# Optimization experiments

Hardware: AMD Instinct MI355X
Metric: run time of the kernel (lower is better)

The kernel has to match this reference:

```python
import jax, jax.numpy as jnp
import numpy as np
from jax import lax

HEADS = 8
DIM_HEAD = 64
INNER = HEADS * DIM_HEAD  # 512
LOG_SCALE_MAX = float(np.log(100.0))  # clamp for clamp_exp (SwinV2-style max temperature 1/0.01)
EPS_NORM = 1e-12  # F.normalize eps
EPS_LN = 1e-5


def setup_inputs() -> dict:
    key = jax.random.key(0)
    ks = jax.random.split(key, 6)
    b, c, h, w = 2, 256, 48, 48
    x = jax.random.normal(ks[0], (b, c, h, w), jnp.float32)
    w_in = jax.random.normal(ks[1], (3 * INNER, c), jnp.float32) * (c ** -0.5)
    b_in = jnp.zeros((3 * INNER,), jnp.float32)
    # learnable log-scale, init log(d_head ** -0.5), per head
    softmax_scale = jnp.full((HEADS, 1, 1), float(np.log(DIM_HEAD ** -0.5)), jnp.float32)
    w_dw = jax.random.normal(ks[2], (INNER, 1, 3, 3), jnp.float32) * (1.0 / 3.0)
    w_pw = jax.random.normal(ks[3], (2 * c, INNER), jnp.float32) * (INNER ** -0.5)
    gamma = jnp.full((2 * c,), 1e-3, jnp.float32)  # norm init_weight=0.001
    beta = jnp.zeros((2 * c,), jnp.float32)
    return {"x": x, "w_in": w_in, "b_in": b_in, "softmax_scale": softmax_scale,
            "w_dw": w_dw, "w_pw": w_pw, "gamma": gamma, "beta": beta}


def _l2norm(t):
    n = jnp.sqrt(jnp.sum(t * t, axis=-1, keepdims=True))
    return t / jnp.maximum(n, EPS_NORM)


def reference(x, w_in, b_in, softmax_scale, w_dw, w_pw, gamma, beta):
    b, c, h, w = x.shape
    s = h * w
    # proj_in: 1x1 conv then 'b (h c) x y -> b h x y c'
    y = jnp.einsum('bchw,oc->bohw', x, w_in) + b_in[None, :, None, None]
    y = y.reshape(b, HEADS, 3 * DIM_HEAD, h, w).transpose(0, 1, 3, 4, 2)  # b H x y (3*dh)
    y = y.reshape(b, HEADS, s, 3 * DIM_HEAD)
    q, k, v = jnp.split(y, 3, axis=-1)  # each [b, H, s, dh]
    # scaled cosine attention
    qn, kn = _l2norm(q), _l2norm(k)
    scale = jnp.exp(jnp.minimum(softmax_scale, LOG_SCALE_MAX))  # clamp_exp, [H,1,1]
    sim = jnp.einsum('bhid,bhjd->bhij', qn, kn) * scale[None]
    attn = jax.nn.softmax(sim, axis=-1)
    out = jnp.einsum('bhij,bhjd->bhid', attn, v)  # [b,H,s,dh]
    # unsplit heads -> 'b (h w) c' -> 'b c h w'
    update = out.transpose(0, 2, 1, 3).reshape(b, s, INNER)
    update = update.transpose(0, 2, 1).reshape(b, INNER, h, w)
    # proj_out: depthwise 3x3 (no bias) + pointwise 1x1 (no bias)
    dw = lax.conv_general_dilated(update, w_dw, (1, 1), 'SAME',
                                  feature_group_count=INNER,
                                  dimension_numbers=('NCHW', 'OIHW', 'NCHW'))
    pw = jnp.einsum('bchw,oc->bohw', dw, w_pw)  # [b, 2c, h, w]
    # channelwise layernorm with small init weight (norm_scales_and_shifts)
    mu = jnp.mean(pw, axis=1, keepdims=True)
    var = jnp.var(pw, axis=1, keepdims=True)
    normed = (pw - mu) * lax.rsqrt(var + EPS_LN)
    normed = normed * gamma[None, :, None, None] + beta[None, :, None, None]
    scales, shifts = jnp.split(normed, 2, axis=1)  # each [b, c, h, w]
    return shifts + x * scales
```

## Files before the change

kernel.cpp:

```cpp
#include <hip/hip_runtime.h>

#define B_ 2
#define C_ 256
#define S_ 2304
#define DH_ 64
#define O3_ 1536
#define INNER_ 512
#define LOGSMAX 4.605170185988092f
#define LOG2E 1.4426950408889634f

typedef __attribute__((ext_vector_type(8))) short short8;
typedef __attribute__((ext_vector_type(4))) float f32x4;
typedef __attribute__((ext_vector_type(16))) float f32x16;
typedef __attribute__((ext_vector_type(4))) unsigned short us4;
typedef __attribute__((ext_vector_type(2))) unsigned u32x2;
typedef __attribute__((ext_vector_type(4))) unsigned u32x4;
typedef __bf16 bf16x8 __attribute__((ext_vector_type(8)));

__device__ __forceinline__ unsigned short f2bf(float f) {
  unsigned u = __builtin_bit_cast(unsigned, f);
  u += 0x7FFFu + ((u >> 16) & 1u);
  return (unsigned short)(u >> 16);
}
__device__ __forceinline__ float bf2f(unsigned short h) {
  return __builtin_bit_cast(float, (unsigned)h << 16);
}
__device__ __forceinline__ bf16x8 as_bf(short8 v) {
  return __builtin_bit_cast(bf16x8, v);
}
__device__ __forceinline__ float fexp2(float x) {
#if __has_builtin(__builtin_amdgcn_exp2f)
  return __builtin_amdgcn_exp2f(x);
#else
  return __expf(x * 0.6931471805599453f);
#endif
}
__device__ __forceinline__ float frcp(float x) {
#if __has_builtin(__builtin_amdgcn_rcpf)
  return __builtin_amdgcn_rcpf(x);
#else
  return 1.f / x;
#endif
}
__device__ __forceinline__ unsigned pack_hi16(unsigned b, unsigned a) {
  return __builtin_amdgcn_perm(b, a, 0x07060302u);
}
__device__ __forceinline__ unsigned pack_lo16(unsigned b, unsigned a) {
  return __builtin_amdgcn_perm(b, a, 0x05040100u);
}

__global__ __launch_bounds__(256) void k_prep(const float* __restrict__ x,
                                              const float* __restrict__ w_in,
                                              const float* __restrict__ w_pw,
                                              unsigned short* __restrict__ xT,
                                              unsigned short* __restrict__ w_inb,
                                              unsigned short* __restrict__ w_pwb) {
  __shared__ float tile[64][65];
  int blk = blockIdx.x;
  int t = threadIdx.x;
  if (blk < 288) {
    int p0 = (blk % 36) * 64, c0 = ((blk / 36) % 4) * 64, b = blk / 144;
    const float* xb = x + (size_t)b * C_ * S_;
#pragma unroll
    for (int i = 0; i < 16; i++) {
      int c = i * 4 + (t >> 6);
      int p = t & 63;
      tile[c][p] = xb[(size_t)(c0 + c) * S_ + p0 + p];
    }
    __syncthreads();
    unsigned short* xTb = xT + (size_t)b * S_ * C_;
#pragma unroll
    for (int i = 0; i < 16; i++) {
      int p = i * 4 + (t >> 6);
      int c = t & 63;
      xTb[(size_t)(p0 + p) * C_ + c0 + c] = f2bf(tile[c][p]);
    }
  } else if (blk < 288 + 1536) {
    int i = (blk - 288) * 256 + t;
    w_inb[i] = f2bf(w_in[i]);
  } else {
    int i = (blk - 1824) * 256 + t;
    w_pwb[i] = f2bf(w_pw[i]);
  }
}

__global__ __launch_bounds__(256) void k_gemm_qkv(const unsigned short* __restrict__ A,
                                                  const unsigned short* __restrict__ BT,
                                                  const float* __restrict__ b_in,
                                                  const float* __restrict__ ss,
                                                  unsigned short* __restrict__ qn,
                                                  unsigned short* __restrict__ kn,
                                                  unsigned short* __restrict__ vv) {
  __shared__ __align__(16) unsigned short As[64][72];
  __shared__ __align__(16) unsigned short Bs[128][72];
  int t = threadIdx.x;
  int lane = t & 63, wv = t >> 6;
  int quad = lane >> 4, r15 = lane & 15;
  int by = blockIdx.y;
  int m0 = by * 64, n0 = blockIdx.x * 128;
  int b = blockIdx.z;
  const unsigned short* BTb = BT + (size_t)b * S_ * C_;

  f32x4 acc[4][2] = {};

  int srA = t >> 2, scA = (t & 3) * 16;
  int srB = t >> 1, scB = (t & 1) * 32;
  const unsigned short* ag = A + (size_t)(m0 + srA) * C_ + scA;
  const unsigned short* bg = BTb + (size_t)(n0 + srB) * C_ + scB;

  for (int k0 = 0; k0 < C_; k0 += 64) {
    short8 a0 = *(const short8*)(ag + k0);
    short8 a1 = *(const short8*)(ag + k0 + 8);
    short8 b0 = *(const short8*)(bg + k0);
    short8 b1 = *(const short8*)(bg + k0 + 8);
    short8 b2 = *(const short8*)(bg + k0 + 16);
    short8 b3 = *(const short8*)(bg + k0 + 24);
    __syncthreads();
    *(short8*)&As[srA][scA] = a0;
    *(short8*)&As[srA][scA + 8] = a1;
    *(short8*)&Bs[srB][scB] = b0;
    *(short8*)&Bs[srB][scB + 8] = b1;
    *(short8*)&Bs[srB][scB + 16] = b2;
    *(short8*)&Bs[srB][scB + 24] = b3;
    __syncthreads();
#pragma unroll
    for (int ks = 0; ks < 2; ks++) {
      short8 af[4], bfr[2];
#pragma unroll
      for (int i = 0; i < 4; i++) af[i] = *(const short8*)&As[i * 16 + r15][ks * 32 + quad * 8];
#pragma unroll
      for (int j = 0; j < 2; j++) bfr[j] = *(const short8*)&Bs[wv * 32 + j * 16 + r15][ks * 32 + quad * 8];
#pragma unroll
      for (int i = 0; i < 4; i++)
#pragma unroll
        for (int j = 0; j < 2; j++)
          acc[i][j] = __builtin_amdgcn_mfma_f32_16x16x32_bf16(as_bf(af[i]), as_bf(bfr[j]), acc[i][j], 0, 0, 0);
    }
  }

  int h = by / 3, seg = by - h * 3;
  int bh = b * 8 + h;
  f32x4 bi[4];
#pragma unroll
  for (int i = 0; i < 4; i++) bi[i] = *(const f32x4*)&b_in[m0 + i * 16 + quad * 4];
  float bv[4][2][4];
  float ssq0 = 0.f, ssq1 = 0.f;
#pragma unroll
  for (int i = 0; i < 4; i++)
#pragma unroll
    for (int rr = 0; rr < 4; rr++) {
      float v0 = acc[i][0][rr] + bi[i][rr];
      float v1 = acc[i][1][rr] + bi[i][rr];
      bv[i][0][rr] = v0;
      bv[i][1][rr] = v1;
      ssq0 += v0 * v0;
      ssq1 += v1 * v1;
    }
  float inv0 = 1.f, inv1 = 1.f;
  if (seg < 2) {
    float sc = (seg == 0) ? __expf(fminf(ss[h], LOGSMAX)) * LOG2E : 1.f;
    ssq0 += __shfl_xor(ssq0, 16);
    ssq0 += __shfl_xor(ssq0, 32);
    ssq1 += __shfl_xor(ssq1, 16);
    ssq1 += __shfl_xor(ssq1, 32);
    inv0 = sc / fmaxf(sqrtf(ssq0), 1e-12f);
    inv1 = sc / fmaxf(sqrtf(ssq1), 1e-12f);
  }
  unsigned short* dst = (seg == 0 ? qn : (seg == 1 ? kn : vv)) + (size_t)bh * S_ * DH_;
#pragma unroll
  for (int i = 0; i < 4; i++)
#pragma unroll
    for (int j = 0; j < 2; j++) {
      float iv = j ? inv1 : inv0;
      us4 o = {f2bf(bv[i][j][0] * iv), f2bf(bv[i][j][1] * iv),
               f2bf(bv[i][j][2] * iv), f2bf(bv[i][j][3] * iv)};
      int p = n0 + wv * 32 + j * 16 + r15;
      *(us4*)&dst[(size_t)p * DH_ + i * 16 + quad * 4] = o;
    }
}

__global__ __launch_bounds__(256) void k_gemm(const unsigned short* __restrict__ A,
                                              const unsigned short* __restrict__ BT,
                                              float* __restrict__ outp,
                                              int M, int N, int K) {
  __shared__ __align__(16) unsigned short As[64][72];
  __shared__ __align__(16) unsigned short Bs[128][72];
  int t = threadIdx.x;
  int lane = t & 63, wv = t >> 6;
  int quad = lane >> 4, r15 = lane & 15;
  int m0 = blockIdx.y * 64, n0 = blockIdx.x * 128;
  int b = blockIdx.z;
  const unsigned short* BTb = BT + (size_t)b * N * K;

  f32x4 acc[4][2] = {};

  int srA = t >> 2, scA = (t & 3) * 16;
  int srB = t >> 1, scB = (t & 1) * 32;
  const unsigned short* ag = A + (size_t)(m0 + srA) * K + scA;
  const unsigned short* bg = BTb + (size_t)(n0 + srB) * K + scB;

  for (int k0 = 0; k0 < K; k0 += 64) {
    short8 a0 = *(const short8*)(ag + k0);
    short8 a1 = *(const short8*)(ag + k0 + 8);
    short8 b0 = *(const short8*)(bg + k0);
    short8 b1 = *(const short8*)(bg + k0 + 8);
    short8 b2 = *(const short8*)(bg + k0 + 16);
    short8 b3 = *(const short8*)(bg + k0 + 24);
    __syncthreads();
    *(short8*)&As[srA][scA] = a0;
    *(short8*)&As[srA][scA + 8] = a1;
    *(short8*)&Bs[srB][scB] = b0;
    *(short8*)&Bs[srB][scB + 8] = b1;
    *(short8*)&Bs[srB][scB + 16] = b2;
    *(short8*)&Bs[srB][scB + 24] = b3;
    __syncthreads();
#pragma unroll
    for (int ks = 0; ks < 2; ks++) {
      short8 af[4], bfr[2];
#pragma unroll
      for (int i = 0; i < 4; i++) af[i] = *(const short8*)&As[i * 16 + r15][ks * 32 + quad * 8];
#pragma unroll
      for (int j = 0; j < 2; j++) bfr[j] = *(const short8*)&Bs[wv * 32 + j * 16 + r15][ks * 32 + quad * 8];
#pragma unroll
      for (int i = 0; i < 4; i++)
#pragma unroll
        for (int j = 0; j < 2; j++)
          acc[i][j] = __builtin_amdgcn_mfma_f32_16x16x32_bf16(as_bf(af[i]), as_bf(bfr[j]), acc[i][j], 0, 0, 0);
    }
  }
  float* Cb = outp + (size_t)b * M * N;
#pragma unroll
  for (int i = 0; i < 4; i++)
#pragma unroll
    for (int j = 0; j < 2; j++)
#pragma unroll
      for (int rr = 0; rr < 4; rr++) {
        int row = m0 + i * 16 + quad * 4 + rr;
        int col = n0 + wv * 32 + j * 16 + r15;
        Cb[(size_t)row * N + col] = acc[i][j][rr];
      }
}

__global__ __launch_bounds__(256) void k_attn(const unsigned short* __restrict__ qn,
                                              const unsigned short* __restrict__ kn,
                                              const unsigned short* __restrict__ vv,
                                              const float* __restrict__ ss,
                                              unsigned short* __restrict__ attnp,
                                              float* __restrict__ lp) {
  __shared__ __align__(16) unsigned short Ks[64][72];
  __shared__ __align__(16) unsigned short Vs[64][72];
  __shared__ __align__(16) unsigned short Ps[4][32][76];
  int t = threadIdx.x;
  int w = t >> 6;
  int lane = t & 63;
  int l31 = lane & 31, hi = lane >> 5;
  int bh = blockIdx.z;
  int q0 = blockIdx.x * 128 + w * 32;
  int split = blockIdx.y;
  int ktbase = split * 12;
  const unsigned short* qb = qn + (size_t)bh * S_ * DH_;
  const unsigned short* kb = kn + (size_t)bh * S_ * DH_;
  const unsigned short* vb = vv + (size_t)bh * S_ * DH_;
  float shift2 = __expf(fminf(ss[bh & 7], LOGSMAX)) * LOG2E;

  const unsigned short* qrow = qb + (size_t)(q0 + l31) * DH_ + hi * 8;
  short8 qf[4];
#pragma unroll
  for (int ks = 0; ks < 4; ks++) qf[ks] = *(const short8*)(qrow + ks * 16);

  const f32x16 z16 = {};
  f32x16 O0 = z16, O1 = z16;
  float l_part = 0.f;

  int srow = t >> 2;
  int scol = (t & 3) * 16;
  const unsigned short* kg = kb + ((size_t)(ktbase * 64) + srow) * DH_ + scol;

  int dp = w * 8 + ((t & 63) >> 3);
  int koct = t & 7;
  const unsigned* vg32 = (const unsigned*)vb + ((size_t)(ktbase * 64 + koct * 8)) * 32 + dp;

  short8 kr0 = *(const short8*)(kg);
  short8 kr1 = *(const short8*)(kg + 8);
  unsigned lv[8];
#pragma unroll
  for (int kk = 0; kk < 8; kk++) lv[kk] = vg32[(size_t)kk * 32];

  for (int i = 0; i < 12; i++) {
    __syncthreads();
    *(short8*)&Ks[srow][scol] = kr0;
    *(short8*)&Ks[srow][scol + 8] = kr1;
    {
      u32x4 ev = {pack_lo16(lv[1], lv[0]), pack_lo16(lv[3], lv[2]),
                  pack_lo16(lv[5], lv[4]), pack_lo16(lv[7], lv[6])};
      u32x4 od = {pack_hi16(lv[1], lv[0]), pack_hi16(lv[3], lv[2]),
                  pack_hi16(lv[5], lv[4]), pack_hi16(lv[7], lv[6])};
      *(u32x4*)&Vs[2 * dp][koct * 8] = ev;
      *(u32x4*)&Vs[2 * dp + 1][koct * 8] = od;
    }
    __syncthreads();
    if (i < 11) {
      size_t koff = (size_t)(i + 1) * 64 * DH_;
      kr0 = *(const short8*)(kg + koff);
      kr1 = *(const short8*)(kg + koff + 8);
      const unsigned* vg = vg32 + (size_t)(i + 1) * 64 * 32;
#pragma unroll
      for (int kk = 0; kk < 8; kk++) lv[kk] = vg[(size_t)kk * 32];
    }
    f32x16 sc0, sc1;
    {
      short8 a0 = *(const short8*)&Ks[l31][hi * 8];
      short8 a1 = *(const short8*)&Ks[32 + l31][hi * 8];
      sc0 = __builtin_amdgcn_mfma_f32_32x32x16_bf16(as_bf(a0), as_bf(qf[0]), z16, 0, 0, 0);
      sc1 = __builtin_amdgcn_mfma_f32_32x32x16_bf16(as_bf(a1), as_bf(qf[0]), z16, 0, 0, 0);
    }
#pragma unroll
    for (int ks = 1; ks < 4; ks++) {
      short8 a0 = *(const short8*)&Ks[l31][ks * 16 + hi * 8];
      short8 a1 = *(const short8*)&Ks[32 + l31][ks * 16 + hi * 8];
      sc0 = __builtin_amdgcn_mfma_f32_32x32x16_bf16(as_bf(a0), as_bf(qf[ks]), sc0, 0, 0, 0);
      sc1 = __builtin_amdgcn_mfma_f32_32x32x16_bf16(as_bf(a1), as_bf(qf[ks]), sc1, 0, 0, 0);
    }
    float lsum = 0.f;
#pragma unroll
    for (int mt = 0; mt < 2; mt++) {
      const f32x16& s = mt ? sc1 : sc0;
#pragma unroll
      for (int g = 0; g < 4; g++) {
        float e0 = fexp2(s[g * 4 + 0] - shift2);
        float e1 = fexp2(s[g * 4 + 1] - shift2);
        float e2 = fexp2(s[g * 4 + 2] - shift2);
        float e3 = fexp2(s[g * 4 + 3] - shift2);
        lsum += (e0 + e1) + (e2 + e3);
        unsigned u0 = __builtin_bit_cast(unsigned, e0) + 0x8000u;
        unsigned u1 = __builtin_bit_cast(unsigned, e1) + 0x8000u;
        unsigned u2 = __builtin_bit_cast(unsigned, e2) + 0x8000u;
        unsigned u3 = __builtin_bit_cast(unsigned, e3) + 0x8000u;
        u32x2 pk = {pack_hi16(u1, u0), pack_hi16(u3, u2)};
        *(u32x2*)&Ps[w][l31][mt * 32 + g * 8 + hi * 4] = pk;
      }
    }
    l_part += lsum;
#pragma unroll
    for (int ks = 0; ks < 4; ks++) {
      short8 pb = *(const short8*)&Ps[w][l31][ks * 16 + hi * 8];
      short8 va0 = *(const short8*)&Vs[l31][ks * 16 + hi * 8];
      short8 va1 = *(const short8*)&Vs[32 + l31][ks * 16 + hi * 8];
      O0 = __builtin_amdgcn_mfma_f32_32x32x16_bf16(as_bf(va0), as_bf(pb), O0, 0, 0, 0);
      O1 = __builtin_amdgcn_mfma_f32_32x32x16_bf16(as_bf(va1), as_bf(pb), O1, 0, 0, 0);
    }
  }
  float l = l_part + __shfl_xor(l_part, 32);
  if (hi == 0) lp[((size_t)(split * 16 + bh)) * S_ + q0 + l31] = l;
  unsigned short* orow = attnp + (((size_t)(split * 16 + bh)) * S_ + q0 + l31) * DH_;
#pragma unroll
  for (int mt = 0; mt < 2; mt++) {
    const f32x16& O = mt ? O1 : O0;
#pragma unroll
    for (int g = 0; g < 4; g++) {
      us4 o4 = {f2bf(O[g * 4 + 0]), f2bf(O[g * 4 + 1]), f2bf(O[g * 4 + 2]), f2bf(O[g * 4 + 3])};
      *(us4*)&orow[mt * 32 + g * 8 + hi * 4] = o4;
    }
  }
}

__global__ __launch_bounds__(256) void k_dwconv(const unsigned short* __restrict__ attnp,
                                                const float* __restrict__ lp,
                                                const float* __restrict__ w_dw,
                                                unsigned short* __restrict__ dwb) {
  int t = threadIdx.x;
  int d = t & 63;
  int pj = t >> 6;
  int p = blockIdx.x * 4 + pj;
  int bh = blockIdx.y;
  int b = bh >> 3, h = bh & 7;
  int yy = p / 48, xx = p % 48;
  const unsigned short* a0 = attnp + (size_t)bh * S_ * DH_ + d;
  const unsigned short* a1 = attnp + ((size_t)(16 + bh)) * S_ * DH_ + d;
  const unsigned short* a2 = attnp + ((size_t)(32 + bh)) * S_ * DH_ + d;
  const float* l0 = lp + (size_t)bh * S_;
  const float* l1 = lp + (size_t)(16 + bh) * S_;
  const float* l2 = lp + (size_t)(32 + bh) * S_;
  int ch = h * 64 + d;
  float w[9];
#pragma unroll
  for (int i = 0; i < 9; i++) w[i] = w_dw[ch * 9 + i];
  float acc = 0.f;
#pragma unroll
  for (int dy = -1; dy <= 1; dy++) {
    int y2 = yy + dy;
    if (y2 < 0 || y2 >= 48) continue;
#pragma unroll
    for (int dx = -1; dx <= 1; dx++) {
      int x2 = xx + dx;
      if (x2 < 0 || x2 >= 48) continue;
      int p2 = y2 * 48 + x2;
      float rl = frcp(l0[p2] + l1[p2] + l2[p2]);
      float v = (bf2f(a0[(size_t)p2 * DH_]) + bf2f(a1[(size_t)p2 * DH_]) + bf2f(a2[(size_t)p2 * DH_])) * rl;
      acc += v * w[(dy + 1) * 3 + dx + 1];
    }
  }
  dwb[((size_t)b * S_ + p) * INNER_ + ch] = f2bf(acc);
}

__global__ __launch_bounds__(256) void k_ln_final(const float* __restrict__ pw,
                                                  const float* __restrict__ gamma,
                                                  const float* __restrict__ beta,
                                                  const float* __restrict__ x,
                                                  float* __restrict__ out) {
  __shared__ float s_s0[32][8], s_s1[32][8], s_q0[32][8], s_q1[32][8];
  int t = threadIdx.x;
  int pl = t & 7, g = t >> 3;
  int b = blockIdx.y;
  int p = blockIdx.x * 16 + pl * 2;
  const float* pwb = pw + (size_t)b * INNER_ * S_ + p;
  float s0 = 0.f, s1 = 0.f, q0 = 0.f, q1 = 0.f;
#pragma unroll
  for (int j = 0; j < 16; j++) {
    float2 v = *(const float2*)&pwb[(size_t)(g * 16 + j) * S_];
    s0 += v.x; s1 += v.y;
    q0 += v.x * v.x; q1 += v.y * v.y;
  }
  s_s0[g][pl] = s0; s_s1[g][pl] = s1;
  s_q0[g][pl] = q0; s_q1[g][pl] = q1;
  __syncthreads();
  float t0 = 0.f, t1 = 0.f, u0 = 0.f, u1 = 0.f;
#pragma unroll
  for (int i = 0; i < 32; i++) {
    t0 += s_s0[i][pl]; t1 += s_s1[i][pl];
    u0 += s_q0[i][pl]; u1 += s_q1[i][pl];
  }
  float mu0 = t0 * (1.f / 512.f), mu1 = t1 * (1.f / 512.f);
  float rs0 = rsqrtf(u0 * (1.f / 512.f) - mu0 * mu0 + 1e-5f);
  float rs1 = rsqrtf(u1 * (1.f / 512.f) - mu1 * mu1 + 1e-5f);
  const float* xb = x + (size_t)b * C_ * S_ + p;
  float* ob = out + (size_t)b * C_ * S_ + p;
#pragma unroll
  for (int j = 0; j < 8; j++) {
    int cc = g * 8 + j;
    float ga = gamma[cc], be = beta[cc];
    float gs = gamma[cc + 256], bs = beta[cc + 256];
    float2 pv = *(const float2*)&pwb[(size_t)cc * S_];
    float2 sv = *(const float2*)&pwb[(size_t)(cc + 256) * S_];
    float2 xv = *(const float2*)&xb[(size_t)cc * S_];
    float sc0 = (pv.x - mu0) * rs0 * ga + be;
    float sc1 = (pv.y - mu1) * rs1 * ga + be;
    float sh0 = (sv.x - mu0) * rs0 * gs + bs;
    float sh1 = (sv.y - mu1) * rs1 * gs + bs;
    float2 o;
    o.x = sh0 + xv.x * sc0;
    o.y = sh1 + xv.y * sc1;
    *(float2*)&ob[(size_t)cc * S_] = o;
  }
}

extern "C" void kernel_launch(void* const* d_in, const int* in_sizes, int n_in,
                              void* d_out, int out_size, void* d_ws, size_t ws_size,
                              hipStream_t stream) {
  const float* x = (const float*)d_in[0];
  const float* w_in = (const float*)d_in[1];
  const float* b_in = (const float*)d_in[2];
  const float* ss = (const float*)d_in[3];
  const float* w_dw = (const float*)d_in[4];
  const float* w_pw = (const float*)d_in[5];
  const float* gamma = (const float*)d_in[6];
  const float* beta = (const float*)d_in[7];
  float* out = (float*)d_out;
  char* ws = (char*)d_ws;

  unsigned short* xT = (unsigned short*)(ws + 0);
  unsigned short* w_inb = (unsigned short*)(ws + 2359296);
  unsigned short* w_pwb = (unsigned short*)(ws + 3145728);
  unsigned short* qn = (unsigned short*)(ws + 3670016);
  unsigned short* kn = (unsigned short*)(ws + 8388608);
  unsigned short* vv = (unsigned short*)(ws + 13107200);
  unsigned short* dwb = (unsigned short*)(ws + 17825792);
  float* lp = (float*)(ws + 22544384);
  unsigned short* attnp = (unsigned short*)(ws + 22986752);
  float* pw = (float*)(ws + 37142528);

  k_prep<<<2848, 256, 0, stream>>>(x, w_in, w_pw, xT, w_inb, w_pwb);
  k_gemm_qkv<<<dim3(18, 24, 2), 256, 0, stream>>>(w_inb, xT, b_in, ss, qn, kn, vv);
  k_attn<<<dim3(18, 3, 16), 256, 0, stream>>>(qn, kn, vv, ss, attnp, lp);
  k_dwconv<<<dim3(576, 16), 256, 0, stream>>>(attnp, lp, w_dw, dwb);
  k_gemm<<<dim3(18, 8, 2), 256, 0, stream>>>(w_pwb, dwb, pw, INNER_, S_, INNER_);
  k_ln_final<<<dim3(144, 2), 256, 0, stream>>>(pw, gamma, beta, x, out);
}
```

Measured before the change: 174.0 us.

## Shrink pointwise GEMM tile to 64x64 and reorder grid axes for attn and dwconv

The pointwise-projection GEMM now uses 64x64 tiles with 128-thread blocks, which doubles the block count (36x8x2) to fill more CUs. The attention and depthwise-conv kernels swap grid dimensions so consecutive block IDs cover different batch-heads, which changes the dispatch order and L2 locality. Smaller GEMM tiles mean less reuse per loaded operand.

```diff
diff --git a/kernel.cpp b/kernel.cpp
--- a/kernel.cpp
+++ b/kernel.cpp
@@ -179,40 +179,43 @@
     }
 }
 
-__global__ __launch_bounds__(256) void k_gemm(const unsigned short* __restrict__ A,
-                                              const unsigned short* __restrict__ BT,
-                                              float* __restrict__ outp,
-                                              int M, int N, int K) {
+__global__ __launch_bounds__(128) void k_gemm2(const unsigned short* __restrict__ A,
+                                               const unsigned short* __restrict__ BT,
+                                               float* __restrict__ outp,
+                                               int M, int N, int K) {
   __shared__ __align__(16) unsigned short As[64][72];
-  __shared__ __align__(16) unsigned short Bs[128][72];
+  __shared__ __align__(16) unsigned short Bs[64][72];
   int t = threadIdx.x;
   int lane = t & 63, wv = t >> 6;
   int quad = lane >> 4, r15 = lane & 15;
-  int m0 = blockIdx.y * 64, n0 = blockIdx.x * 128;
+  int m0 = blockIdx.y * 64, n0 = blockIdx.x * 64;
   int b = blockIdx.z;
   const unsigned short* BTb = BT + (size_t)b * N * K;
 
   f32x4 acc[4][2] = {};
 
-  int srA = t >> 2, scA = (t & 3) * 16;
-  int srB = t >> 1, scB = (t & 1) * 32;
-  const unsigned short* ag = A + (size_t)(m0 + srA) * K + scA;
-  const unsigned short* bg = BTb + (size_t)(n0 + srB) * K + scB;
+  int sr = t >> 1, sc = (t & 1) * 32;
+  const unsigned short* ag = A + (size_t)(m0 + sr) * K + sc;
+  const unsigned short* bg = BTb + (size_t)(n0 + sr) * K + sc;
 
   for (int k0 = 0; k0 < K; k0 += 64) {
     short8 a0 = *(const short8*)(ag + k0);
     short8 a1 = *(const short8*)(ag + k0 + 8);
+    short8 a2 = *(const short8*)(ag + k0 + 16);
+    short8 a3 = *(const short8*)(ag + k0 + 24);
     short8 b0 = *(const short8*)(bg + k0);
     short8 b1 = *(const short8*)(bg + k0 + 8);
     short8 b2 = *(const short8*)(bg + k0 + 16);
     short8 b3 = *(const short8*)(bg + k0 + 24);
     __syncthreads();
-    *(short8*)&As[srA][scA] = a0;
-    *(short8*)&As[srA][scA + 8] = a1;
-    *(short8*)&Bs[srB][scB] = b0;
-    *(short8*)&Bs[srB][scB + 8] = b1;
-    *(short8*)&Bs[srB][scB + 16] = b2;
-    *(short8*)&Bs[srB][scB + 24] = b3;
+    *(short8*)&As[sr][sc] = a0;
+    *(short8*)&As[sr][sc + 8] = a1;
+    *(short8*)&As[sr][sc + 16] = a2;
+    *(short8*)&As[sr][sc + 24] = a3;
+    *(short8*)&Bs[sr][sc] = b0;
+    *(short8*)&Bs[sr][sc + 8] = b1;
+    *(short8*)&Bs[sr][sc + 16] = b2;
+    *(short8*)&Bs[sr][sc + 24] = b3;
     __syncthreads();
 #pragma unroll
     for (int ks = 0; ks < 2; ks++) {
@@ -254,9 +257,9 @@
   int w = t >> 6;
   int lane = t & 63;
   int l31 = lane & 31, hi = lane >> 5;
-  int bh = blockIdx.z;
-  int q0 = blockIdx.x * 128 + w * 32;
-  int split = blockIdx.y;
+  int bh = blockIdx.x;
+  int q0 = blockIdx.y * 128 + w * 32;
+  int split = blockIdx.z;
   int ktbase = split * 12;
   const unsigned short* qb = qn + (size_t)bh * S_ * DH_;
   const unsigned short* kb = kn + (size_t)bh * S_ * DH_;
@@ -371,8 +374,8 @@
   int t = threadIdx.x;
   int d = t & 63;
   int pj = t >> 6;
-  int p = blockIdx.x * 4 + pj;
-  int bh = blockIdx.y;
+  int p = blockIdx.y * 4 + pj;
+  int bh = blockIdx.x;
   int b = bh >> 3, h = bh & 7;
   int yy = p / 48, xx = p % 48;
   const unsigned short* a0 = attnp + (size_t)bh * S_ * DH_ + d;
@@ -481,8 +484,8 @@
 
   k_prep<<<2848, 256, 0, stream>>>(x, w_in, w_pw, xT, w_inb, w_pwb);
   k_gemm_qkv<<<dim3(18, 24, 2), 256, 0, stream>>>(w_inb, xT, b_in, ss, qn, kn, vv);
-  k_attn<<<dim3(18, 3, 16), 256, 0, stream>>>(qn, kn, vv, ss, attnp, lp);
-  k_dwconv<<<dim3(576, 16), 256, 0, stream>>>(attnp, lp, w_dw, dwb);
-  k_gemm<<<dim3(18, 8, 2), 256, 0, stream>>>(w_pwb, dwb, pw, INNER_, S_, INNER_);
+  k_attn<<<dim3(16, 18, 3), 256, 0, stream>>>(qn, kn, vv, ss, attnp, lp);
+  k_dwconv<<<dim3(16, 576), 256, 0, stream>>>(attnp, lp, w_dw, dwb);
+  k_gemm2<<<dim3(36, 8, 2), 128, 0, stream>>>(w_pwb, dwb, pw, INNER_, S_, INNER_);
   k_ln_final<<<dim3(144, 2), 256, 0, stream>>>(pw, gamma, beta, x, out);
 }
```

Measured after the change: 171.9 us. Within noise of the previous version (-1.2%).
